# Kernel tuning notes

Hardware: AMD Instinct MI355X
Metric: run time of the kernel (lower is better)

## Reference

```python
import jax, jax.numpy as jnp
import numpy as np

N_NODES = 100000

def gcn_conv(x, W, b, src, dst, deg_isqrt):
    # x: [N, Fin] -> lin -> [N, Fout]; aggregate src->dst with sym norm; + bias
    h = x @ W                                   # [N, Fout]
    norm = deg_isqrt[src] * deg_isqrt[dst]      # [E+N]
    msg = h[src] * norm[:, None]                # [E+N, Fout]
    out = jax.ops.segment_sum(msg, dst, num_segments=N_NODES)
    return out + b

def setup_inputs() -> dict:
    key = jax.random.key(0)
    k1, k2, k3, k4 = jax.random.split(key, 4)
    x = jax.random.normal(k1, (N_NODES, 256), dtype=jnp.float32)
    edge_index = jax.random.randint(k2, (2, 3200000), 0, N_NODES, dtype=jnp.int32)
    # Glorot-ish params for GCNConv(256->16) and GCNConv(16->1)
    W1 = jax.random.normal(k3, (256, 16), dtype=jnp.float32) * (1.0 / np.sqrt(256))
    b1 = jnp.zeros((16,), dtype=jnp.float32)
    W2 = jax.random.normal(k4, (16, 1), dtype=jnp.float32) * (1.0 / np.sqrt(16))
    b2 = jnp.zeros((1,), dtype=jnp.float32)
    return {"x": x, "edge_index": edge_index, "W1": W1, "b1": b1, "W2": W2, "b2": b2}

def reference(x, edge_index, W1, b1, W2, b2):
    # GCNConv adds self-loops then symmetric normalization deg^{-1/2}
    loops = jnp.arange(N_NODES, dtype=edge_index.dtype)
    src = jnp.concatenate([edge_index[0], loops])
    dst = jnp.concatenate([edge_index[1], loops])
    deg = jax.ops.segment_sum(jnp.ones_like(src, dtype=x.dtype), dst, num_segments=N_NODES)
    deg_isqrt = jnp.where(deg > 0, jax.lax.rsqrt(deg), 0.0)

    h = gcn_conv(x, W1, b1, src, dst, deg_isqrt)
    h = jax.nn.relu(h)
    # dropout(p=0.5, train=self.training): eval mode -> identity (deterministic reference)
    out = gcn_conv(h, W2, b2, src, dst, deg_isqrt)
    return out  # [N, 1]
```

## Files before the change

kernel.cpp:

```cpp
#include <hip/hip_runtime.h>
#include <hip/hip_fp16.h>


#define SBSH 8
#define SBCAP 10240
#define LCAP 9216
#define HPAD 400
#define GSTR 16
#define BINTHREADS 1024
#define ITEMS 8

__global__ void k_init(int* __restrict__ gcur, int Bsb) {
    int i = blockIdx.x * blockDim.x + threadIdx.x;
    if (i < Bsb) gcur[i * GSTR] = i * SBCAP;
}

__global__ __launch_bounds__(BINTHREADS) void k_p1(
    const int* __restrict__ src, const int* __restrict__ dst,
    int* __restrict__ gcur, int* __restrict__ pairs, int E, int Bsb)
{
    __shared__ int hist[HPAD];
    const int t = threadIdx.x;
    const int base4 = blockIdx.x * (BINTHREADS * ITEMS / 4);
    for (int i = t; i < HPAD; i += BINTHREADS) hist[i] = 0;
    __syncthreads();

    int4 dd[ITEMS / 4];
    #pragma unroll
    for (int r = 0; r < ITEMS / 4; ++r) {
        const int i4 = base4 + r * BINTHREADS + t;
        const int i = i4 << 2;
        int4 v;
        if (i + 3 < E) v = ((const int4*)dst)[i4];
        else {
            v.x = (i     < E) ? dst[i]     : -1;
            v.y = (i + 1 < E) ? dst[i + 1] : -1;
            v.z = (i + 2 < E) ? dst[i + 2] : -1;
            v.w = (i + 3 < E) ? dst[i + 3] : -1;
        }
        dd[r] = v;
        if (v.x >= 0) atomicAdd(&hist[v.x >> SBSH], 1);
        if (v.y >= 0) atomicAdd(&hist[v.y >> SBSH], 1);
        if (v.z >= 0) atomicAdd(&hist[v.z >> SBSH], 1);
        if (v.w >= 0) atomicAdd(&hist[v.w >> SBSH], 1);
    }
    __syncthreads();
    for (int i = t; i < Bsb; i += BINTHREADS) {
        int c = hist[i];
        hist[i] = c ? atomicAdd(&gcur[i * GSTR], c) : 0;
    }
    __syncthreads();
    #pragma unroll
    for (int r = 0; r < ITEMS / 4; ++r) {
        const int i4 = base4 + r * BINTHREADS + t;
        const int i = i4 << 2;
        int4 s;
        if (i + 3 < E) s = ((const int4*)src)[i4];
        else {
            s.x = (i     < E) ? src[i]     : 0;
            s.y = (i + 1 < E) ? src[i + 1] : 0;
            s.z = (i + 2 < E) ? src[i + 2] : 0;
            s.w = (i + 3 < E) ? src[i + 3] : 0;
        }
        int4 v = dd[r];
        if (v.x >= 0) { int p = atomicAdd(&hist[v.x >> SBSH], 1); pairs[p] = (s.x << SBSH) | (v.x & 255); }
        if (v.y >= 0) { int p = atomicAdd(&hist[v.y >> SBSH], 1); pairs[p] = (s.y << SBSH) | (v.y & 255); }
        if (v.z >= 0) { int p = atomicAdd(&hist[v.z >> SBSH], 1); pairs[p] = (s.z << SBSH) | (v.z & 255); }
        if (v.w >= 0) { int p = atomicAdd(&hist[v.w >> SBSH], 1); pairs[p] = (s.w << SBSH) | (v.w & 255); }
    }
}

__global__ __launch_bounds__(1024) void k_sortsb(
    int* __restrict__ pairs, const int* __restrict__ gcur,
    int* __restrict__ rowp, float* __restrict__ isq, int N)
{
    __shared__ int e[LCAP];
    __shared__ int s2[LCAP];
    __shared__ int hist[256];
    __shared__ int cur[256];
    __shared__ int wsum[4];
    const int t = threadIdx.x, sb = blockIdx.x;
    const int beg = sb * SBCAP;
    int cnt = gcur[sb * GSTR] - beg;
    if (cnt > LCAP) cnt = LCAP;
    if (t < 256) hist[t] = 0;
    __syncthreads();
    const int c4 = cnt >> 2;
    {
        const int4* p4 = (const int4*)(pairs + beg);
        int4* e4 = (int4*)e;
        for (int i = t; i < c4; i += 1024) {
            int4 v = p4[i];
            e4[i] = v;
            atomicAdd(&hist[v.x & 255], 1);
            atomicAdd(&hist[v.y & 255], 1);
            atomicAdd(&hist[v.z & 255], 1);
            atomicAdd(&hist[v.w & 255], 1);
        }
        for (int i = (c4 << 2) + t; i < cnt; i += 1024) {
            int p = pairs[beg + i];
            e[i] = p;
            atomicAdd(&hist[p & 255], 1);
        }
    }
    __syncthreads();
    int c = 0, v = 0;
    if (t < 256) {
        const int lane = t & 63, w = t >> 6;
        c = hist[t];
        v = c;
        #pragma unroll
        for (int off = 1; off < 64; off <<= 1) {
            int u = __shfl_up(v, off, 64);
            if (lane >= off) v += u;
        }
        if (lane == 63) wsum[w] = v;
    }
    __syncthreads();
    if (t < 256) {
        const int w = t >> 6;
        int add = 0;
        #pragma unroll
        for (int i = 0; i < 3; ++i) if (i < w) add += wsum[i];
        int inc = v + add;
        int exc = inc - c;
        cur[t] = exc;
        rowp[sb * 257 + t] = exc;
        if (t == 255) rowp[sb * 257 + 256] = inc;
        int n = (sb << SBSH) + t;
        if (n < N) isq[n] = rsqrtf((float)(c + 1));
    }
    __syncthreads();
    for (int i = t; i < cnt; i += 1024) {
        int p = e[i];
        int pos = atomicAdd(&cur[p & 255], 1);
        s2[pos] = p >> SBSH;
    }
    __syncthreads();
    {
        int4* p4 = (int4*)(pairs + beg);
        const int4* s4 = (const int4*)s2;
        for (int i = t; i < c4; i += 1024) p4[i] = s4[i];
        for (int i = (c4 << 2) + t; i < cnt; i += 1024) pairs[beg + i] = s2[i];
    }
}

__global__ __launch_bounds__(256) void k_lin1(
    const float* __restrict__ x, const float* __restrict__ W1,
    const float* __restrict__ isq, __half* __restrict__ hs16, int N)
{
    __shared__ float part[128][16];
    const int t = threadIdx.x;
    const int w = t >> 6, lane = t & 63;
    const int hu = __builtin_amdgcn_readfirstlane(w >> 1);
    const int nl = ((w & 1) << 6) + lane;
    const int n = blockIdx.x * 128 + nl;
    const int nc = (n < N) ? n : (N - 1);
    const float4* xr = (const float4*)(x + ((size_t)nc << 8) + (hu << 7));
    float acc[16];
    #pragma unroll
    for (int f = 0; f < 16; ++f) acc[f] = 0.f;
    #pragma unroll 1
    for (int kb = 0; kb < 4; ++kb) {
        float4 xa[8];
        #pragma unroll
        for (int u = 0; u < 8; ++u) xa[u] = xr[(kb << 3) + u];
        #pragma unroll
        for (int u = 0; u < 8; ++u) {
            const int k4 = (kb << 3) + u;
            const float4* wr = (const float4*)W1 + (hu << 9) + (k4 << 4);
            const float xv[4] = { xa[u].x, xa[u].y, xa[u].z, xa[u].w };
            #pragma unroll
            for (int j = 0; j < 4; ++j) {
                #pragma unroll
                for (int f4 = 0; f4 < 4; ++f4) {
                    const float4 wv = wr[(j << 2) + f4];
                    acc[(f4 << 2) + 0] = fmaf(xv[j], wv.x, acc[(f4 << 2) + 0]);
                    acc[(f4 << 2) + 1] = fmaf(xv[j], wv.y, acc[(f4 << 2) + 1]);
                    acc[(f4 << 2) + 2] = fmaf(xv[j], wv.z, acc[(f4 << 2) + 2]);
                    acc[(f4 << 2) + 3] = fmaf(xv[j], wv.w, acc[(f4 << 2) + 3]);
                }
            }
        }
    }
    if (hu == 1) {
        #pragma unroll
        for (int f4 = 0; f4 < 4; ++f4) {
            const int fs = (f4 ^ (nl & 3)) << 2;
            *(float4*)&part[nl][fs] =
                make_float4(acc[(f4 << 2) + 0], acc[(f4 << 2) + 1],
                            acc[(f4 << 2) + 2], acc[(f4 << 2) + 3]);
        }
    }
    __syncthreads();
    if (hu == 0 && n < N) {
        #pragma unroll
        for (int f4 = 0; f4 < 4; ++f4) {
            const int fs = (f4 ^ (nl & 3)) << 2;
            float4 p = *(const float4*)&part[nl][fs];
            acc[(f4 << 2) + 0] += p.x;
            acc[(f4 << 2) + 1] += p.y;
            acc[(f4 << 2) + 2] += p.z;
            acc[(f4 << 2) + 3] += p.w;
        }
        const float iq = isq[n];
        __half2* o = (__half2*)&hs16[(size_t)n << 4];
        #pragma unroll
        for (int f2 = 0; f2 < 8; ++f2)
            o[f2] = __floats2half2_rn(acc[2 * f2] * iq, acc[2 * f2 + 1] * iq);
    }
}

__global__ __launch_bounds__(256) void k_agg1(
    const int* __restrict__ sorted, const int* __restrict__ rowp,
    const __half* __restrict__ hs16, const float* __restrict__ isq,
    const float* __restrict__ b1, const float* __restrict__ W2,
    float* __restrict__ ts, int N)
{
    const int t = threadIdx.x, g = blockIdx.x;
    const int l = t >> 3, q = t & 3, p = (t >> 2) & 1;
    const int n = g * 32 + l;
    if (n >= N) return;
    const int sb = n >> SBSH, L = n & 255;
    const int rbeg = sb * SBCAP + rowp[sb * 257 + L];
    const int rend = sb * SBCAP + rowp[sb * 257 + L + 1];
    const float2* h2 = (const float2*)hs16;
    float a0 = 0.f, a1 = 0.f, a2 = 0.f, a3 = 0.f;
    for (int j = rbeg + p; j < rend; j += 2) {
        int s0 = sorted[j];
        float2 ra = h2[s0 * 4 + q];
        union { float f; __half2 h; } ca0, ca1;
        ca0.f = ra.x; ca1.f = ra.y;
        float2 fa0 = __half22float2(ca0.h), fa1 = __half22float2(ca1.h);
        a0 += fa0.x; a1 += fa0.y; a2 += fa1.x; a3 += fa1.y;
    }
    a0 += __shfl_xor(a0, 4);
    a1 += __shfl_xor(a1, 4);
    a2 += __shfl_xor(a2, 4);
    a3 += __shfl_xor(a3, 4);
    {
        float2 rs = h2[(size_t)n * 4 + q];
        union { float f; __half2 h; } c0, c1;
        c0.f = rs.x; c1.f = rs.y;
        float2 f0 = __half22float2(c0.h), f1 = __half22float2(c1.h);
        a0 += f0.x; a1 += f0.y; a2 += f1.x; a3 += f1.y;
    }
    const float iq = isq[n];
    const int f0i = q * 4;
    float pr = fmaxf(a0 * iq + b1[f0i + 0], 0.f) * W2[f0i + 0]
             + fmaxf(a1 * iq + b1[f0i + 1], 0.f) * W2[f0i + 1]
             + fmaxf(a2 * iq + b1[f0i + 2], 0.f) * W2[f0i + 2]
             + fmaxf(a3 * iq + b1[f0i + 3], 0.f) * W2[f0i + 3];
    pr += __shfl_xor(pr, 1);
    pr += __shfl_xor(pr, 2);
    if ((t & 7) == 0) ts[n] = pr * iq;
}

__global__ __launch_bounds__(256) void k_agg2(
    const int* __restrict__ sorted, const int* __restrict__ rowp,
    const float* __restrict__ ts, const float* __restrict__ isq,
    const float* __restrict__ b2, float* __restrict__ out, int N)
{
    const int t = threadIdx.x;
    const int l = t >> 3, q = t & 7;
    const int n = blockIdx.x * 32 + l;
    if (n >= N) return;
    const int sb = n >> SBSH, L = n & 255;
    const int rbeg = sb * SBCAP + rowp[sb * 257 + L];
    const int rend = sb * SBCAP + rowp[sb * 257 + L + 1];
    float acc = 0.f;
    for (int j = rbeg + q; j < rend; j += 8) acc += ts[sorted[j]];
    acc += __shfl_xor(acc, 1);
    acc += __shfl_xor(acc, 2);
    acc += __shfl_xor(acc, 4);
    if (q == 0) out[n] = (acc + ts[n]) * isq[n] + b2[0];
}

extern "C" void kernel_launch(void* const* d_in, const int* in_sizes, int n_in,
                              void* d_out, int out_size, void* d_ws, size_t ws_size,
                              hipStream_t stream) {
    const float* x  = (const float*)d_in[0];
    const int*   ei = (const int*)d_in[1];
    const float* W1 = (const float*)d_in[2];
    const float* b1 = (const float*)d_in[3];
    const float* W2 = (const float*)d_in[4];
    const float* b2 = (const float*)d_in[5];
    const int N = in_sizes[0] / 256;
    const int E = in_sizes[1] / 2;
    const int* src = ei;
    const int* dst = ei + E;
    const int Bsb = (N + 255) >> SBSH;

    char* w = (char*)d_ws;
    float*  isq   = (float*)w;  w += (size_t)N * 4;
    int*    gcur  = (int*)w;    w += (size_t)HPAD * GSTR * 4;
    int*    pairs = (int*)w;    w += (size_t)Bsb * SBCAP * 4;
    int*    rowp  = (int*)w;    w += (size_t)Bsb * 257 * 4;
    __half* hs16  = (__half*)w; w += (size_t)N * 32;
    float*  ts    = (float*)w;  w += (size_t)N * 4;
    float*  out   = (float*)d_out;

    k_init<<<(Bsb + 255) / 256, 256, 0, stream>>>(gcur, Bsb);

    const int nbBin = (E + BINTHREADS * ITEMS - 1) / (BINTHREADS * ITEMS);
    k_p1<<<nbBin, BINTHREADS, 0, stream>>>(src, dst, gcur, pairs, E, Bsb);

    k_sortsb<<<Bsb, 1024, 0, stream>>>(pairs, gcur, rowp, isq, N);

    k_lin1<<<(N + 127) / 128, 256, 0, stream>>>(x, W1, isq, hs16, N);

    k_agg1<<<(N + 31) / 32, 256, 0, stream>>>(pairs, rowp, hs16, isq, b1, W2, ts, N);
    k_agg2<<<(N + 31) / 32, 256, 0, stream>>>(pairs, rowp, ts, isq, b2, out, N);
}
```

Baseline: 277.1 us.

## Replace per-superbucket counting sort with LDS atomic scatter aggregation

```diff
diff --git a/kernel.cpp b/kernel.cpp
--- a/kernel.cpp
+++ b/kernel.cpp
@@ -4,7 +4,6 @@
 
 #define SBSH 8
 #define SBCAP 10240
-#define LCAP 9216
 #define HPAD 400
 #define GSTR 16
 #define BINTHREADS 1024
@@ -70,78 +69,31 @@
     }
 }
 
-__global__ __launch_bounds__(1024) void k_sortsb(
-    int* __restrict__ pairs, const int* __restrict__ gcur,
-    int* __restrict__ rowp, float* __restrict__ isq, int N)
-{
-    __shared__ int e[LCAP];
-    __shared__ int s2[LCAP];
+__global__ __launch_bounds__(1024) void k_deg(
+    const int* __restrict__ pairs, const int* __restrict__ gcur,
+    float* __restrict__ isq, int N)
+{
     __shared__ int hist[256];
-    __shared__ int cur[256];
-    __shared__ int wsum[4];
     const int t = threadIdx.x, sb = blockIdx.x;
     const int beg = sb * SBCAP;
-    int cnt = gcur[sb * GSTR] - beg;
-    if (cnt > LCAP) cnt = LCAP;
+    const int cnt = gcur[sb * GSTR] - beg;
     if (t < 256) hist[t] = 0;
     __syncthreads();
     const int c4 = cnt >> 2;
-    {
-        const int4* p4 = (const int4*)(pairs + beg);
-        int4* e4 = (int4*)e;
-        for (int i = t; i < c4; i += 1024) {
-            int4 v = p4[i];
-            e4[i] = v;
-            atomicAdd(&hist[v.x & 255], 1);
-            atomicAdd(&hist[v.y & 255], 1);
-            atomicAdd(&hist[v.z & 255], 1);
-            atomicAdd(&hist[v.w & 255], 1);
-        }
-        for (int i = (c4 << 2) + t; i < cnt; i += 1024) {
-            int p = pairs[beg + i];
-            e[i] = p;
-            atomicAdd(&hist[p & 255], 1);
-        }
-    }
-    __syncthreads();
-    int c = 0, v = 0;
+    const int4* p4 = (const int4*)(pairs + beg);
+    for (int i = t; i < c4; i += 1024) {
+        int4 v = p4[i];
+        atomicAdd(&hist[v.x & 255], 1);
+        atomicAdd(&hist[v.y & 255], 1);
+        atomicAdd(&hist[v.z & 255], 1);
+        atomicAdd(&hist[v.w & 255], 1);
+    }
+    for (int i = (c4 << 2) + t; i < cnt; i += 1024)
+        atomicAdd(&hist[pairs[beg + i] & 255], 1);
+    __syncthreads();
     if (t < 256) {
-        const int lane = t & 63, w = t >> 6;
-        c = hist[t];
-        v = c;
-        #pragma unroll
-        for (int off = 1; off < 64; off <<= 1) {
-            int u = __shfl_up(v, off, 64);
-            if (lane >= off) v += u;
-        }
-        if (lane == 63) wsum[w] = v;
-    }
-    __syncthreads();
-    if (t < 256) {
-        const int w = t >> 6;
-        int add = 0;
-        #pragma unroll
-        for (int i = 0; i < 3; ++i) if (i < w) add += wsum[i];
-        int inc = v + add;
-        int exc = inc - c;
-        cur[t] = exc;
-        rowp[sb * 257 + t] = exc;
-        if (t == 255) rowp[sb * 257 + 256] = inc;
-        int n = (sb << SBSH) + t;
-        if (n < N) isq[n] = rsqrtf((float)(c + 1));
-    }
-    __syncthreads();
-    for (int i = t; i < cnt; i += 1024) {
-        int p = e[i];
-        int pos = atomicAdd(&cur[p & 255], 1);
-        s2[pos] = p >> SBSH;
-    }
-    __syncthreads();
-    {
-        int4* p4 = (int4*)(pairs + beg);
-        const int4* s4 = (const int4*)s2;
-        for (int i = t; i < c4; i += 1024) p4[i] = s4[i];
-        for (int i = (c4 << 2) + t; i < cnt; i += 1024) pairs[beg + i] = s2[i];
+        const int n = (sb << SBSH) + t;
+        if (n < N) isq[n] = rsqrtf((float)(hist[t] + 1));
     }
 }
 
@@ -211,69 +163,94 @@
     }
 }
 
-__global__ __launch_bounds__(256) void k_agg1(
-    const int* __restrict__ sorted, const int* __restrict__ rowp,
+__global__ __launch_bounds__(1024) void k_agg1f(
+    const int* __restrict__ pairs, const int* __restrict__ gcur,
     const __half* __restrict__ hs16, const float* __restrict__ isq,
     const float* __restrict__ b1, const float* __restrict__ W2,
     float* __restrict__ ts, int N)
 {
-    const int t = threadIdx.x, g = blockIdx.x;
-    const int l = t >> 3, q = t & 3, p = (t >> 2) & 1;
-    const int n = g * 32 + l;
-    if (n >= N) return;
-    const int sb = n >> SBSH, L = n & 255;
-    const int rbeg = sb * SBCAP + rowp[sb * 257 + L];
-    const int rend = sb * SBCAP + rowp[sb * 257 + L + 1];
-    const float2* h2 = (const float2*)hs16;
-    float a0 = 0.f, a1 = 0.f, a2 = 0.f, a3 = 0.f;
-    for (int j = rbeg + p; j < rend; j += 2) {
-        int s0 = sorted[j];
-        float2 ra = h2[s0 * 4 + q];
-        union { float f; __half2 h; } ca0, ca1;
-        ca0.f = ra.x; ca1.f = ra.y;
-        float2 fa0 = __half22float2(ca0.h), fa1 = __half22float2(ca1.h);
-        a0 += fa0.x; a1 += fa0.y; a2 += fa1.x; a3 += fa1.y;
-    }
-    a0 += __shfl_xor(a0, 4);
-    a1 += __shfl_xor(a1, 4);
-    a2 += __shfl_xor(a2, 4);
-    a3 += __shfl_xor(a3, 4);
-    {
-        float2 rs = h2[(size_t)n * 4 + q];
-        union { float f; __half2 h; } c0, c1;
-        c0.f = rs.x; c1.f = rs.y;
-        float2 f0 = __half22float2(c0.h), f1 = __half22float2(c1.h);
-        a0 += f0.x; a1 += f0.y; a2 += f1.x; a3 += f1.y;
-    }
-    const float iq = isq[n];
-    const int f0i = q * 4;
-    float pr = fmaxf(a0 * iq + b1[f0i + 0], 0.f) * W2[f0i + 0]
-             + fmaxf(a1 * iq + b1[f0i + 1], 0.f) * W2[f0i + 1]
-             + fmaxf(a2 * iq + b1[f0i + 2], 0.f) * W2[f0i + 2]
-             + fmaxf(a3 * iq + b1[f0i + 3], 0.f) * W2[f0i + 3];
-    pr += __shfl_xor(pr, 1);
-    pr += __shfl_xor(pr, 2);
-    if ((t & 7) == 0) ts[n] = pr * iq;
-}
-
-__global__ __launch_bounds__(256) void k_agg2(
-    const int* __restrict__ sorted, const int* __restrict__ rowp,
+    __shared__ float facc[256 * 16];
+    const int t = threadIdx.x, sb = blockIdx.x;
+    const int beg = sb * SBCAP;
+    const int cnt = gcur[sb * GSTR] - beg;
+    #pragma unroll
+    for (int i = t; i < 4096; i += 1024) facc[i] = 0.f;
+    __syncthreads();
+    for (int i = t; i < cnt; i += 1024) {
+        const int p = pairs[beg + i];
+        const int s = p >> SBSH, d = p & 255;
+        const int r = (d >> 1) & 15;
+        float* fb = &facc[d << 4];
+        union { float4 v; __half2 h[4]; } U0, U1;
+        const float4* hr = (const float4*)(hs16 + ((size_t)s << 4));
+        U0.v = hr[0];
+        U1.v = hr[1];
+        #pragma unroll
+        for (int c = 0; c < 4; ++c) {
+            float2 f2 = __half22float2(U0.h[c]);
+            atomicAdd(&fb[(2 * c)     ^ r], f2.x);
+            atomicAdd(&fb[(2 * c + 1) ^ r], f2.y);
+        }
+        #pragma unroll
+        for (int c = 0; c < 4; ++c) {
+            float2 f2 = __half22float2(U1.h[c]);
+            atomicAdd(&fb[(8 + 2 * c) ^ r], f2.x);
+            atomicAdd(&fb[(9 + 2 * c) ^ r], f2.y);
+        }
+    }
+    __syncthreads();
+    if (t < 256) {
+        const int n = (sb << SBSH) + t;
+        if (n < N) {
+            const float iq = isq[n];
+            const int r = (t >> 1) & 15;
+            const float* fb = &facc[t << 4];
+            union { float4 v; __half2 h[4]; } S0, S1;
+            const float4* hr = (const float4*)(hs16 + ((size_t)n << 4));
+            S0.v = hr[0];
+            S1.v = hr[1];
+            float acc = 0.f;
+            #pragma unroll
+            for (int c = 0; c < 4; ++c) {
+                float2 sf = __half22float2(S0.h[c]);
+                float a0 = fb[(2 * c)     ^ r] + sf.x;
+                float a1 = fb[(2 * c + 1) ^ r] + sf.y;
+                acc += fmaxf(a0 * iq + b1[2 * c],     0.f) * W2[2 * c]
+                     + fmaxf(a1 * iq + b1[2 * c + 1], 0.f) * W2[2 * c + 1];
+            }
+            #pragma unroll
+            for (int c = 0; c < 4; ++c) {
+                float2 sf = __half22float2(S1.h[c]);
+                float a0 = fb[(8 + 2 * c) ^ r] + sf.x;
+                float a1 = fb[(9 + 2 * c) ^ r] + sf.y;
+                acc += fmaxf(a0 * iq + b1[8 + 2 * c], 0.f) * W2[8 + 2 * c]
+                     + fmaxf(a1 * iq + b1[9 + 2 * c], 0.f) * W2[9 + 2 * c];
+            }
+            ts[n] = acc * iq;
+        }
+    }
+}
+
+__global__ __launch_bounds__(1024) void k_agg2f(
+    const int* __restrict__ pairs, const int* __restrict__ gcur,
     const float* __restrict__ ts, const float* __restrict__ isq,
     const float* __restrict__ b2, float* __restrict__ out, int N)
 {
-    const int t = threadIdx.x;
-    const int l = t >> 3, q = t & 7;
-    const int n = blockIdx.x * 32 + l;
-    if (n >= N) return;
-    const int sb = n >> SBSH, L = n & 255;
-    const int rbeg = sb * SBCAP + rowp[sb * 257 + L];
-    const int rend = sb * SBCAP + rowp[sb * 257 + L + 1];
-    float acc = 0.f;
-    for (int j = rbeg + q; j < rend; j += 8) acc += ts[sorted[j]];
-    acc += __shfl_xor(acc, 1);
-    acc += __shfl_xor(acc, 2);
-    acc += __shfl_xor(acc, 4);
-    if (q == 0) out[n] = (acc + ts[n]) * isq[n] + b2[0];
+    __shared__ float sacc[256];
+    const int t = threadIdx.x, sb = blockIdx.x;
+    const int beg = sb * SBCAP;
+    const int cnt = gcur[sb * GSTR] - beg;
+    if (t < 256) sacc[t] = 0.f;
+    __syncthreads();
+    for (int i = t; i < cnt; i += 1024) {
+        const int p = pairs[beg + i];
+        atomicAdd(&sacc[p & 255], ts[p >> SBSH]);
+    }
+    __syncthreads();
+    if (t < 256) {
+        const int n = (sb << SBSH) + t;
+        if (n < N) out[n] = (sacc[t] + ts[n]) * isq[n] + b2[0];
+    }
 }
 
 extern "C" void kernel_launch(void* const* d_in, const int* in_sizes, int n_in,
@@ -295,7 +272,6 @@
     float*  isq   = (float*)w;  w += (size_t)N * 4;
     int*    gcur  = (int*)w;    w += (size_t)HPAD * GSTR * 4;
     int*    pairs = (int*)w;    w += (size_t)Bsb * SBCAP * 4;
-    int*    rowp  = (int*)w;    w += (size_t)Bsb * 257 * 4;
     __half* hs16  = (__half*)w; w += (size_t)N * 32;
     float*  ts    = (float*)w;  w += (size_t)N * 4;
     float*  out   = (float*)d_out;
@@ -305,10 +281,10 @@
     const int nbBin = (E + BINTHREADS * ITEMS - 1) / (BINTHREADS * ITEMS);
     k_p1<<<nbBin, BINTHREADS, 0, stream>>>(src, dst, gcur, pairs, E, Bsb);
 
-    k_sortsb<<<Bsb, 1024, 0, stream>>>(pairs, gcur, rowp, isq, N);
+    k_deg<<<Bsb, 1024, 0, stream>>>(pairs, gcur, isq, N);
 
     k_lin1<<<(N + 127) / 128, 256, 0, stream>>>(x, W1, isq, hs16, N);
 
-    k_agg1<<<(N + 31) / 32, 256, 0, stream>>>(pairs, rowp, hs16, isq, b1, W2, ts, N);
-    k_agg2<<<(N + 31) / 32, 256, 0, stream>>>(pairs, rowp, ts, isq, b2, out, N);
-}
+    k_agg1f<<<Bsb, 1024, 0, stream>>>(pairs, gcur, hs16, isq, b1, W2, ts, N);
+    k_agg2f<<<Bsb, 1024, 0, stream>>>(pairs, gcur, ts, isq, b2, out, N);
+}
```

Result: slower. 580.3 us (+109.4%).

## Stage binned edges in LDS for coalesced scatter and keep sort ranks in registers

Applied to the files above, without the earlier changes.

```diff
diff --git a/kernel.cpp b/kernel.cpp
--- a/kernel.cpp
+++ b/kernel.cpp
@@ -7,66 +7,93 @@
 #define LCAP 9216
 #define HPAD 400
 #define GSTR 16
-#define BINTHREADS 1024
-#define ITEMS 8
+#define PEDG 8192
 
 __global__ void k_init(int* __restrict__ gcur, int Bsb) {
     int i = blockIdx.x * blockDim.x + threadIdx.x;
     if (i < Bsb) gcur[i * GSTR] = i * SBCAP;
 }
 
-__global__ __launch_bounds__(BINTHREADS) void k_p1(
+__global__ __launch_bounds__(1024) void k_p1(
     const int* __restrict__ src, const int* __restrict__ dst,
     int* __restrict__ gcur, int* __restrict__ pairs, int E, int Bsb)
 {
-    __shared__ int hist[HPAD];
+    __shared__ int s2[PEDG];
+    __shared__ unsigned short rid[PEDG];
+    __shared__ int hist[392];
+    __shared__ int loc[392];
+    __shared__ int gbase[392];
+    __shared__ int wsum[8];
     const int t = threadIdx.x;
-    const int base4 = blockIdx.x * (BINTHREADS * ITEMS / 4);
-    for (int i = t; i < HPAD; i += BINTHREADS) hist[i] = 0;
-    __syncthreads();
-
-    int4 dd[ITEMS / 4];
-    #pragma unroll
-    for (int r = 0; r < ITEMS / 4; ++r) {
-        const int i4 = base4 + r * BINTHREADS + t;
+    const int base4 = blockIdx.x * (PEDG / 4);
+    for (int i = t; i < 392; i += 1024) hist[i] = 0;
+    __syncthreads();
+
+    int4 dd[2], ss[2], rk[2];
+    #pragma unroll
+    for (int r = 0; r < 2; ++r) {
+        const int i4 = base4 + r * 1024 + t;
         const int i = i4 << 2;
-        int4 v;
-        if (i + 3 < E) v = ((const int4*)dst)[i4];
-        else {
+        int4 v, s;
+        if (i + 3 < E) {
+            v = ((const int4*)dst)[i4];
+            s = ((const int4*)src)[i4];
+        } else {
             v.x = (i     < E) ? dst[i]     : -1;
             v.y = (i + 1 < E) ? dst[i + 1] : -1;
             v.z = (i + 2 < E) ? dst[i + 2] : -1;
             v.w = (i + 3 < E) ? dst[i + 3] : -1;
-        }
-        dd[r] = v;
-        if (v.x >= 0) atomicAdd(&hist[v.x >> SBSH], 1);
-        if (v.y >= 0) atomicAdd(&hist[v.y >> SBSH], 1);
-        if (v.z >= 0) atomicAdd(&hist[v.z >> SBSH], 1);
-        if (v.w >= 0) atomicAdd(&hist[v.w >> SBSH], 1);
-    }
-    __syncthreads();
-    for (int i = t; i < Bsb; i += BINTHREADS) {
-        int c = hist[i];
-        hist[i] = c ? atomicAdd(&gcur[i * GSTR], c) : 0;
-    }
-    __syncthreads();
-    #pragma unroll
-    for (int r = 0; r < ITEMS / 4; ++r) {
-        const int i4 = base4 + r * BINTHREADS + t;
-        const int i = i4 << 2;
-        int4 s;
-        if (i + 3 < E) s = ((const int4*)src)[i4];
-        else {
             s.x = (i     < E) ? src[i]     : 0;
             s.y = (i + 1 < E) ? src[i + 1] : 0;
             s.z = (i + 2 < E) ? src[i + 2] : 0;
             s.w = (i + 3 < E) ? src[i + 3] : 0;
         }
-        int4 v = dd[r];
-        if (v.x >= 0) { int p = atomicAdd(&hist[v.x >> SBSH], 1); pairs[p] = (s.x << SBSH) | (v.x & 255); }
-        if (v.y >= 0) { int p = atomicAdd(&hist[v.y >> SBSH], 1); pairs[p] = (s.y << SBSH) | (v.y & 255); }
-        if (v.z >= 0) { int p = atomicAdd(&hist[v.z >> SBSH], 1); pairs[p] = (s.z << SBSH) | (v.z & 255); }
-        if (v.w >= 0) { int p = atomicAdd(&hist[v.w >> SBSH], 1); pairs[p] = (s.w << SBSH) | (v.w & 255); }
+        dd[r] = v; ss[r] = s;
+        int4 q = make_int4(0, 0, 0, 0);
+        if (v.x >= 0) q.x = atomicAdd(&hist[v.x >> SBSH], 1);
+        if (v.y >= 0) q.y = atomicAdd(&hist[v.y >> SBSH], 1);
+        if (v.z >= 0) q.z = atomicAdd(&hist[v.z >> SBSH], 1);
+        if (v.w >= 0) q.w = atomicAdd(&hist[v.w >> SBSH], 1);
+        rk[r] = q;
+    }
+    __syncthreads();
+    int c = 0, vv = 0;
+    if (t < 391) {
+        const int lane = t & 63, w = t >> 6;
+        c = hist[t];
+        vv = c;
+        #pragma unroll
+        for (int off = 1; off < 64; off <<= 1) {
+            int u = __shfl_up(vv, off, 64);
+            if (lane >= off) vv += u;
+        }
+        if (lane == 63 || t == 390) wsum[w] = vv;
+    }
+    __syncthreads();
+    if (t < 391) {
+        const int w = t >> 6;
+        int add = 0;
+        #pragma unroll
+        for (int i = 0; i < 6; ++i) if (i < w) add += wsum[i];
+        int inc = vv + add, exc = inc - c;
+        loc[t] = exc;
+        if (t == 390) loc[391] = inc;
+        gbase[t] = c ? atomicAdd(&gcur[t * GSTR], c) : 0;
+    }
+    __syncthreads();
+    const int tot = loc[391];
+    #pragma unroll
+    for (int r = 0; r < 2; ++r) {
+        int4 v = dd[r], s = ss[r], q = rk[r];
+        if (v.x >= 0) { int sb = v.x >> SBSH; int p = loc[sb] + q.x; s2[p] = (s.x << SBSH) | (v.x & 255); rid[p] = (unsigned short)sb; }
+        if (v.y >= 0) { int sb = v.y >> SBSH; int p = loc[sb] + q.y; s2[p] = (s.y << SBSH) | (v.y & 255); rid[p] = (unsigned short)sb; }
+        if (v.z >= 0) { int sb = v.z >> SBSH; int p = loc[sb] + q.z; s2[p] = (s.z << SBSH) | (v.z & 255); rid[p] = (unsigned short)sb; }
+        if (v.w >= 0) { int sb = v.w >> SBSH; int p = loc[sb] + q.w; s2[p] = (s.w << SBSH) | (v.w & 255); rid[p] = (unsigned short)sb; }
+    }
+    __syncthreads();
+    for (int i = t; i < tot; i += 1024) {
+        const int sb = rid[i];
+        pairs[gbase[sb] + (i - loc[sb])] = s2[i];
     }
 }
 
@@ -74,10 +101,9 @@
     int* __restrict__ pairs, const int* __restrict__ gcur,
     int* __restrict__ rowp, float* __restrict__ isq, int N)
 {
-    __shared__ int e[LCAP];
     __shared__ int s2[LCAP];
     __shared__ int hist[256];
-    __shared__ int cur[256];
+    __shared__ int exc[256];
     __shared__ int wsum[4];
     const int t = threadIdx.x, sb = blockIdx.x;
     const int beg = sb * SBCAP;
@@ -86,22 +112,24 @@
     if (t < 256) hist[t] = 0;
     __syncthreads();
     const int c4 = cnt >> 2;
+    const int4* p4 = (const int4*)(pairs + beg);
+    int4 va[3], ra[3];
+    int vr = 0, rr = 0;
+    #pragma unroll
+    for (int k = 0; k < 3; ++k) {
+        const int i = t + k * 1024;
+        if (i < c4) {
+            int4 v = p4[i];
+            va[k] = v;
+            ra[k].x = atomicAdd(&hist[v.x & 255], 1);
+            ra[k].y = atomicAdd(&hist[v.y & 255], 1);
+            ra[k].z = atomicAdd(&hist[v.z & 255], 1);
+            ra[k].w = atomicAdd(&hist[v.w & 255], 1);
+        }
+    }
     {
-        const int4* p4 = (const int4*)(pairs + beg);
-        int4* e4 = (int4*)e;
-        for (int i = t; i < c4; i += 1024) {
-            int4 v = p4[i];
-            e4[i] = v;
-            atomicAdd(&hist[v.x & 255], 1);
-            atomicAdd(&hist[v.y & 255], 1);
-            atomicAdd(&hist[v.z & 255], 1);
-            atomicAdd(&hist[v.w & 255], 1);
-        }
-        for (int i = (c4 << 2) + t; i < cnt; i += 1024) {
-            int p = pairs[beg + i];
-            e[i] = p;
-            atomicAdd(&hist[p & 255], 1);
-        }
+        const int i = (c4 << 2) + t;
+        if (i < cnt) { vr = pairs[beg + i]; rr = atomicAdd(&hist[vr & 255], 1); }
     }
     __syncthreads();
     int c = 0, v = 0;
@@ -123,24 +151,34 @@
         #pragma unroll
         for (int i = 0; i < 3; ++i) if (i < w) add += wsum[i];
         int inc = v + add;
-        int exc = inc - c;
-        cur[t] = exc;
-        rowp[sb * 257 + t] = exc;
+        int e0 = inc - c;
+        exc[t] = e0;
+        rowp[sb * 257 + t] = e0;
         if (t == 255) rowp[sb * 257 + 256] = inc;
         int n = (sb << SBSH) + t;
         if (n < N) isq[n] = rsqrtf((float)(c + 1));
     }
     __syncthreads();
-    for (int i = t; i < cnt; i += 1024) {
-        int p = e[i];
-        int pos = atomicAdd(&cur[p & 255], 1);
-        s2[pos] = p >> SBSH;
-    }
-    __syncthreads();
+    #pragma unroll
+    for (int k = 0; k < 3; ++k) {
+        const int i = t + k * 1024;
+        if (i < c4) {
+            int4 v2 = va[k], q = ra[k];
+            s2[exc[v2.x & 255] + q.x] = v2.x >> SBSH;
+            s2[exc[v2.y & 255] + q.y] = v2.y >> SBSH;
+            s2[exc[v2.z & 255] + q.z] = v2.z >> SBSH;
+            s2[exc[v2.w & 255] + q.w] = v2.w >> SBSH;
+        }
+    }
     {
-        int4* p4 = (int4*)(pairs + beg);
+        const int i = (c4 << 2) + t;
+        if (i < cnt) s2[exc[vr & 255] + rr] = vr >> SBSH;
+    }
+    __syncthreads();
+    {
+        int4* pw = (int4*)(pairs + beg);
         const int4* s4 = (const int4*)s2;
-        for (int i = t; i < c4; i += 1024) p4[i] = s4[i];
+        for (int i = t; i < c4; i += 1024) pw[i] = s4[i];
         for (int i = (c4 << 2) + t; i < cnt; i += 1024) pairs[beg + i] = s2[i];
     }
 }
@@ -302,8 +340,8 @@
 
     k_init<<<(Bsb + 255) / 256, 256, 0, stream>>>(gcur, Bsb);
 
-    const int nbBin = (E + BINTHREADS * ITEMS - 1) / (BINTHREADS * ITEMS);
-    k_p1<<<nbBin, BINTHREADS, 0, stream>>>(src, dst, gcur, pairs, E, Bsb);
+    const int nbBin = (E + PEDG - 1) / PEDG;
+    k_p1<<<nbBin, 1024, 0, stream>>>(src, dst, gcur, pairs, E, Bsb);
 
     k_sortsb<<<Bsb, 1024, 0, stream>>>(pairs, gcur, rowp, isq, N);
 
```

Result: faster. 260.8 us (-5.9%).
